# Optimization experiments

Measured on AMD Instinct MI355X. Metric: run time of the kernel, lower is better.

## Reference

```python
import jax, jax.numpy as jnp
import numpy as np

N = 512       # n_nodes (also number of per-node attention heads)
F_IN = 256    # n_feature
H = 64        # h_feature
C = 64        # n_class (must equal H for V * out broadcast)
K = 12        # top-K threshold for learned adjacency
ALPHA = 0.2   # LeakyReLU negative slope


def setup_inputs() -> dict:
    key = jax.random.key(0)
    ks = jax.random.split(key, 6)
    X = jax.random.normal(ks[0], (N, F_IN), jnp.float32)
    # stacked params of the n_nodes first-layer attention heads
    W_stack = jax.random.normal(ks[1], (N, F_IN, H), jnp.float32) * 0.05
    a_stack = jax.random.normal(ks[2], (N, 2 * H, 1), jnp.float32) * 0.05
    # output attention layer: in_Channel = h_feature * n_nodes
    W_out = jax.random.normal(ks[3], (H * N, C), jnp.float32) * 0.02
    a_out = jax.random.normal(ks[4], (2 * C, 1), jnp.float32) * 0.05
    V = jax.random.normal(ks[5], (N, H), jnp.float32) * 0.1
    return {"X": X, "W_stack": W_stack, "a_stack": a_stack,
            "W_out": W_out, "a_out": a_out, "V": V}


def gat_layer(Hx, adj, W, a):
    # Faithful to Graph_Attention_Covlayer.forward, but the O(N^2 * 2F)
    # concat tensor is algebraically collapsed: concat(Wh[i], Wh[j]) @ a
    # == (Wh @ a1)[i] + (Wh @ a2)[j], a broadcast sum.
    Wh = Hx @ W                      # (N, F)
    f = W.shape[1]
    e1 = Wh @ a[:f, 0]               # (N,)
    e2 = Wh @ a[f:, 0]               # (N,)
    S = jax.nn.leaky_relu(e1[:, None] + e2[None, :], ALPHA)  # (N, N)
    A = jax.nn.softmax(S, axis=1)    # softmax BEFORE masking, as in source
    A = jnp.where(adj > 0, A, jnp.zeros_like(A))
    out = A @ Wh                     # (N, F)
    return jax.nn.elu(out)           # concat=True -> elu


def adj_learn(V):
    A = V @ V.T                      # (N, N)
    kth = jax.lax.top_k(A.reshape(-1), K)[0][-1]
    # source: Adj = 1 where A > kth-value, else 0 (strict >)
    return jnp.where(A > kth, jnp.ones_like(A), jnp.zeros_like(A))


def reference(X, W_stack, a_stack, W_out, a_out, V):
    adj = adj_learn(V)
    # all n_nodes heads share input X and adj -> vmap over stacked params
    heads = jax.vmap(lambda W, a: gat_layer(X, adj, W, a))(W_stack, a_stack)  # (N_heads, N, H)
    # torch.cat(..., dim=1): row i = [head0_feats | head1_feats | ...]
    mid = jnp.transpose(heads, (1, 0, 2)).reshape(N, N * H)
    # dropout: eval mode -> identity
    out = gat_layer(mid, adj, W_out, a_out)  # (N, C)
    out = jax.nn.elu(V * out)
    return adj, out
```

## Files before the change

kernel.cpp:

```cpp
#include <hip/hip_runtime.h>


#define CAND_OFF 0
#define XT_OFF   12288
#define KTH_OFF  143360
#define INT_OFF  143424
#define MIDC_OFF 143488
#define PART_OFF 536704

#define H_M    0
#define H_R    1
#define H_ROWS 2
#define H_ER   14
#define H_EJ   26
#define H_ECJ  38

__device__ __forceinline__ float leaky_(float x) { return fmaxf(x, 0.2f * x); }
__device__ __forceinline__ float elu_(float x)   { return x > 0.f ? x : __expf(x) - 1.f; }

__global__ __launch_bounds__(256) void k1_prep(const float* __restrict__ V,
                                               const float* __restrict__ X,
                                               float* __restrict__ wsf,
                                               float* __restrict__ out) {
  int b = blockIdx.x, t = threadIdx.x, l = t & 63, w = t >> 6;
  if (b < 512) {
    __shared__ float vi[64];
    __shared__ float redv[4]; __shared__ int redi[4];
    __shared__ float candv[12]; __shared__ int candi[12];
    if (t < 64) vi[t] = V[b * 64 + t];
    __syncthreads();
    float vr0, vr1;
    {
      const float4* vj = reinterpret_cast<const float4*>(V + t * 64);
      float acc = 0.f;
      #pragma unroll
      for (int q = 0; q < 16; ++q) {
        float4 v4 = vj[q];
        acc += v4.x * vi[q*4] + v4.y * vi[q*4+1] + v4.z * vi[q*4+2] + v4.w * vi[q*4+3];
      }
      vr0 = acc;
    }
    {
      const float4* vj = reinterpret_cast<const float4*>(V + (t + 256) * 64);
      float acc = 0.f;
      #pragma unroll
      for (int q = 0; q < 16; ++q) {
        float4 v4 = vj[q];
        acc += v4.x * vi[q*4] + v4.y * vi[q*4+1] + v4.z * vi[q*4+2] + v4.w * vi[q*4+3];
      }
      vr1 = acc;
    }
    out[b * 512 + t]       = vr0;
    out[b * 512 + 256 + t] = vr1;
    if (b < 128) out[262144 + b * 256 + t] = 0.f;

    float v0 = vr0, v1 = vr1;
    int j0 = t, j1 = t + 256;
    for (int round = 0; round < 12; ++round) {
      float m; int mi;
      if (v0 >= v1) { m = v0; mi = j0; } else { m = v1; mi = j1; }
      #pragma unroll
      for (int d = 1; d < 64; d <<= 1) {
        float ov = __shfl_xor(m, d);
        int   oi = __shfl_xor(mi, d);
        if (ov > m || (ov == m && oi < mi)) { m = ov; mi = oi; }
      }
      if (l == 0) { redv[w] = m; redi[w] = mi; }
      __syncthreads();
      float bm = redv[0]; int bi = redi[0];
      #pragma unroll
      for (int ww = 1; ww < 4; ++ww)
        if (redv[ww] > bm || (redv[ww] == bm && redi[ww] < bi)) { bm = redv[ww]; bi = redi[ww]; }
      if (t == 0) { candv[round] = bm; candi[round] = bi; }
      if (bi == j0) v0 = -INFINITY;
      if (bi == j1) v1 = -INFINITY;
      __syncthreads();
    }
    if (t < 12) {
      float2 c; c.x = candv[t]; c.y = __int_as_float(b * 512 + candi[t]);
      *reinterpret_cast<float2*>(wsf + CAND_OFF + (b * 12 + t) * 2) = c;
    }
  } else {
    __shared__ float tile[64][65];
    int ti = b - 512;
    int tjj = ti & 7;
    int tff = ti >> 3;
    int r = t >> 2, c0 = (t & 3) * 16;
    #pragma unroll
    for (int u = 0; u < 4; ++u) {
      float4 x4 = *reinterpret_cast<const float4*>(X + (tjj*64 + r)*256 + tff*64 + c0 + u*4);
      tile[c0+u*4+0][r] = x4.x; tile[c0+u*4+1][r] = x4.y;
      tile[c0+u*4+2][r] = x4.z; tile[c0+u*4+3][r] = x4.w;
    }
    __syncthreads();
    int fl = t >> 2, jc0 = (t & 3) * 16;
    #pragma unroll
    for (int u = 0; u < 4; ++u) {
      float4 o4 = make_float4(tile[fl][jc0+u*4+0], tile[fl][jc0+u*4+1],
                              tile[fl][jc0+u*4+2], tile[fl][jc0+u*4+3]);
      *reinterpret_cast<float4*>(wsf + XT_OFF + (tff*64 + fl)*512 + tjj*64 + jc0 + u*4) = o4;
    }
  }
}

__global__ void k2_header(float* __restrict__ wsf) {
  __shared__ float redv[4]; __shared__ int redi[4];
  __shared__ float candv[12]; __shared__ int candi[12];
  __shared__ int es_s[12], rows_s[12];
  __shared__ int M_s, R_s;
  int t = threadIdx.x, l = t & 63, w = t >> 6;

  float v[24]; int ix[24];
  const float2* cp = reinterpret_cast<const float2*>(wsf + CAND_OFF);
  #pragma unroll
  for (int k = 0; k < 24; ++k) {
    float2 c = cp[k * 256 + t];
    v[k] = c.x; ix[k] = __float_as_int(c.y);
  }
  unsigned rm = 0;
  for (int round = 0; round < 12; ++round) {
    float m = -INFINITY; int mi = 0x7FFFFFFF; int sel = -1;
    #pragma unroll
    for (int k = 0; k < 24; ++k) {
      bool ok = ((rm >> k) & 1u) == 0u;
      bool better = ok && (v[k] > m || (v[k] == m && ix[k] < mi));
      if (better) { m = v[k]; mi = ix[k]; sel = k; }
    }
    float lm = m; int lmi = mi; (void)lm;
    #pragma unroll
    for (int d = 1; d < 64; d <<= 1) {
      float ov = __shfl_xor(m, d);
      int   oi = __shfl_xor(mi, d);
      if (ov > m || (ov == m && oi < mi)) { m = ov; mi = oi; }
    }
    if (l == 0) { redv[w] = m; redi[w] = mi; }
    __syncthreads();
    float bm = redv[0]; int bi = redi[0];
    #pragma unroll
    for (int ww = 1; ww < 4; ++ww)
      if (redv[ww] > bm || (redv[ww] == bm && redi[ww] < bi)) { bm = redv[ww]; bi = redi[ww]; }
    if (t == 0) { candv[round] = bm; candi[round] = bi; }
    if (sel >= 0 && lmi == bi) rm |= 1u << sel;
    __syncthreads();
  }

  float kv = candv[11];
  bool valid = (t < 12) && (candv[t] > kv);
  int myidx = valid ? candi[t] : 0x7FFFFFFF;
  unsigned long long vm = __ballot(valid);
  if (t < 12) {
    int rank = 0;
    #pragma unroll
    for (int q = 0; q < 12; ++q)
      if (((vm >> q) & 1ull) && candi[q] < myidx) ++rank;
    if (valid) es_s[rank] = myidx;
    if (t == 0) M_s = (int)__popcll(vm & 0xFFFull);
  }
  __syncthreads();
  int M = M_s;
  bool isent = (t < M);
  int i2 = isent ? (es_s[t] >> 9) : -1;
  int j2 = isent ? (es_s[t] & 511) : 0;
  bool isnew = isent && (t == 0 || (es_s[t - 1] >> 9) != i2);
  unsigned long long nm = __ballot(isnew);
  if (isnew) {
    int r = (int)__popcll(nm & ((1ull << t) - 1ull));
    rows_s[r] = i2;
  }
  if (t == 0) R_s = (int)__popcll(nm & 0xFFFull);
  __syncthreads();
  int R = R_s;
  int* ip = (int*)(wsf + INT_OFF);
  if (t == 0) { ip[H_M] = M; ip[H_R] = R; wsf[KTH_OFF] = kv; }
  if (t < 12) {
    ip[H_ROWS + t] = (t < R) ? rows_s[t] : 0;
    int er = 0, ecj = -1;
    if (isent) {
      er = (int)__popcll(nm & ((2ull << t) - 1ull)) - 1;
      for (int r = 0; r < R; ++r) if (rows_s[r] == j2) ecj = r;
    }
    ip[H_ER + t]  = er;
    ip[H_EJ + t]  = isent ? j2 : 0;
    ip[H_ECJ + t] = ecj;
  }
}

__global__ __launch_bounds__(256) void k3_heads(
    const float* __restrict__ X, const float* __restrict__ Wst,
    const float* __restrict__ ast, float* __restrict__ wsf,
    float* __restrict__ out) {
  __shared__ int   shdr[64];
  __shared__ __align__(16) float XeT[3072];
  __shared__ __align__(16) float whp[3072];
  __shared__ float w1l[256], w2l[256];
  __shared__ float e2s[512];
  __shared__ float whl[768];
  __shared__ float e1r[12], mr12[12], sr12[12], av12[12];
  __shared__ float redv[4], redf[48];

  int b = blockIdx.x, t = threadIdx.x, l = t & 63, w = t >> 6;
  const int* ip = (const int*)(wsf + INT_OFF);

  {
    float kv = wsf[KTH_OFF];
    float a0 = out[b * 512 + t], a1 = out[b * 512 + 256 + t];
    out[b * 512 + t]       = (a0 > kv) ? 1.f : 0.f;
    out[b * 512 + 256 + t] = (a1 > kv) ? 1.f : 0.f;
  }
  if (t < 50) shdr[t] = ip[t];
  __syncthreads();
  int M = shdr[H_M], R = shdr[H_R];

  #pragma unroll
  for (int m = 0; m < 12; ++m) {
    float v = 0.f;
    if (m < M) v = X[shdr[H_EJ + m] * 256 + t];
    XeT[t * 12 + m] = v;
  }
  __syncthreads();

  const float* Wb = Wst + b * 16384;
  int fg = l >> 4, kc = (l & 15) << 2;
  float4 a1q = *reinterpret_cast<const float4*>(ast + b * 128 + kc);
  float4 a2q = *reinterpret_cast<const float4*>(ast + b * 128 + 64 + kc);
  float wh[12][4];
  #pragma unroll
  for (int m = 0; m < 12; ++m) { wh[m][0] = wh[m][1] = wh[m][2] = wh[m][3] = 0.f; }

  #pragma unroll 4
  for (int it = 0; it < 16; ++it) {
    int f = w * 64 + it * 4 + fg;
    float4 wq = *reinterpret_cast<const float4*>(Wb + f * 64 + kc);
    float p1 = wq.x*a1q.x + wq.y*a1q.y + wq.z*a1q.z + wq.w*a1q.w;
    float p2 = wq.x*a2q.x + wq.y*a2q.y + wq.z*a2q.z + wq.w*a2q.w;
    #pragma unroll
    for (int d = 1; d < 16; d <<= 1) { p1 += __shfl_xor(p1, d); p2 += __shfl_xor(p2, d); }
    if ((l & 15) == 0) { w1l[f] = p1; w2l[f] = p2; }
    const float4* xr = reinterpret_cast<const float4*>(&XeT[f * 12]);
    float4 xa = xr[0], xb = xr[1], xc = xr[2];
    float xv[12] = { xa.x, xa.y, xa.z, xa.w, xb.x, xb.y, xb.z, xb.w,
                     xc.x, xc.y, xc.z, xc.w };
    #pragma unroll
    for (int m = 0; m < 12; ++m) {
      wh[m][0] += xv[m] * wq.x;
      wh[m][1] += xv[m] * wq.y;
      wh[m][2] += xv[m] * wq.z;
      wh[m][3] += xv[m] * wq.w;
    }
  }
  #pragma unroll
  for (int m = 0; m < 12; ++m) {
    #pragma unroll
    for (int q = 0; q < 4; ++q) {
      float x = wh[m][q];
      x += __shfl_xor(x, 16);
      x += __shfl_xor(x, 32);
      wh[m][q] = x;
    }
  }
  if (l < 16) {
    #pragma unroll
    for (int m = 0; m < 12; ++m) {
      float4 vv = make_float4(wh[m][0], wh[m][1], wh[m][2], wh[m][3]);
      *reinterpret_cast<float4*>(&whp[w * 768 + m * 64 + kc]) = vv;
    }
  }
  __syncthreads();
  #pragma unroll
  for (int c = 0; c < 3; ++c) {
    int o = c * 256 + t;
    whl[o] = whp[o] + whp[768 + o] + whp[1536 + o] + whp[2304 + o];
  }
  for (int r = w; r < R; r += 4) {
    int row = shdr[H_ROWS + r];
    float p = 0.f;
    #pragma unroll
    for (int s = 0; s < 4; ++s) {
      int f = s * 64 + l;
      p += X[row * 256 + f] * w1l[f];
    }
    #pragma unroll
    for (int d = 1; d < 64; d <<= 1) p += __shfl_xor(p, d);
    if (l == 0) e1r[r] = p;
  }
  {
    const float2* XT2 = reinterpret_cast<const float2*>(wsf + XT_OFF);
    float a0 = 0.f, a1 = 0.f;
    #pragma unroll 8
    for (int f = 0; f < 256; ++f) {
      float2 xv = XT2[f * 256 + t];
      float wf = w2l[f];
      a0 += xv.x * wf; a1 += xv.y * wf;
    }
    e2s[2 * t] = a0; e2s[2 * t + 1] = a1;
  }
  __syncthreads();

  {
    float p = fmaxf(e2s[w * 128 + l], e2s[w * 128 + 64 + l]);
    #pragma unroll
    for (int d = 1; d < 64; d <<= 1) p = fmaxf(p, __shfl_xor(p, d));
    if (l == 0) redv[w] = p;
  }
  __syncthreads();
  float maxe2 = fmaxf(fmaxf(redv[0], redv[1]), fmaxf(redv[2], redv[3]));
  for (int r = 0; r < R; ++r) {
    float e1_ = e1r[r];
    float m_ = leaky_(e1_ + maxe2);
    float pe = __expf(leaky_(e1_ + e2s[t]) - m_) + __expf(leaky_(e1_ + e2s[t + 256]) - m_);
    #pragma unroll
    for (int d = 1; d < 64; d <<= 1) pe += __shfl_xor(pe, d);
    if (l == 0) redf[r * 4 + w] = pe;
    if (t == r) mr12[r] = m_;
  }
  __syncthreads();
  if (t < R) sr12[t] = redf[t * 4] + redf[t * 4 + 1] + redf[t * 4 + 2] + redf[t * 4 + 3];
  __syncthreads();
  if (t < M) {
    int r = shdr[H_ER + t];
    av12[t] = __expf(leaky_(e1r[r] + e2s[shdr[H_EJ + t]]) - mr12[r]) / sr12[r];
  }
  __syncthreads();
  for (int r = w; r < R; r += 4) {
    float a = 0.f;
    #pragma unroll
    for (int m = 0; m < 12; ++m) {
      if (m < M && shdr[H_ER + m] == r) a += av12[m] * whl[m * 64 + l];
    }
    wsf[MIDC_OFF + r * 32768 + b * 64 + l] = elu_(a);
  }
}

__global__ void k4_wh2(const float* __restrict__ Wout, float* __restrict__ wsf) {
  __shared__ __align__(16) float midT[256 * 12];
  __shared__ float whp[4][768];
  int b = blockIdx.x, t = threadIdx.x;
  int l = t & 63, w = t >> 6;
  const int* ip = (const int*)(wsf + INT_OFF);
  int R = ip[H_R];
  #pragma unroll
  for (int m = 0; m < 12; ++m) {
    float v = 0.f;
    if (m < R) v = wsf[MIDC_OFF + m * 32768 + b * 256 + t];
    midT[t * 12 + m] = v;
  }
  __syncthreads();
  float acc[12];
  #pragma unroll
  for (int m = 0; m < 12; ++m) acc[m] = 0.f;
  #pragma unroll 2
  for (int ci = 0; ci < 64; ++ci) {
    int cc = w * 64 + ci;
    float wv = Wout[(b * 256 + cc) * 64 + l];
    const float4* xr = reinterpret_cast<const float4*>(&midT[cc * 12]);
    float4 xa = xr[0], xb = xr[1], xc = xr[2];
    acc[0] += xa.x * wv; acc[1] += xa.y * wv; acc[2]  += xa.z * wv; acc[3]  += xa.w * wv;
    acc[4] += xb.x * wv; acc[5] += xb.y * wv; acc[6]  += xb.z * wv; acc[7]  += xb.w * wv;
    acc[8] += xc.x * wv; acc[9] += xc.y * wv; acc[10] += xc.z * wv; acc[11] += xc.w * wv;
  }
  #pragma unroll
  for (int m = 0; m < 12; ++m) whp[w][m * 64 + l] = acc[m];
  __syncthreads();
  #pragma unroll
  for (int c = 0; c < 3; ++c) {
    int o = c * 256 + t;
    float s = whp[0][o] + whp[1][o] + whp[2][o] + whp[3][o];
    wsf[PART_OFF + b * 768 + o] = s;
  }
}

__global__ void k5_final(const float* __restrict__ aout, const float* __restrict__ V,
                         float* __restrict__ wsf, float* __restrict__ out) {
  __shared__ float Wh2[768];
  __shared__ float e1o[12], e2o[12], mr[12], sr[12], avals[12];
  int t = threadIdx.x;
  const int* ip = (const int*)(wsf + INT_OFF);
  int M = ip[H_M], R = ip[H_R];
  for (int o = t, c = 0; c < 3; ++c, o += 256) {
    float s = 0.f;
    #pragma unroll 8
    for (int bb = 0; bb < 128; ++bb) s += wsf[PART_OFF + bb * 768 + o];
    Wh2[o] = s;
  }
  __syncthreads();
  if (t < R) {
    float s1 = 0.f, s2 = 0.f;
    for (int k = 0; k < 64; ++k) {
      float wv = Wh2[t * 64 + k];
      s1 += wv * aout[k];
      s2 += wv * aout[64 + k];
    }
    e1o[t] = s1; e2o[t] = s2;
  }
  __syncthreads();
  if (t < R) {
    float maxe = 0.f;
    for (int r = 0; r < R; ++r) maxe = fmaxf(maxe, e2o[r]);
    float m_ = leaky_(e1o[t] + maxe);
    float s = (float)(512 - R) * __expf(leaky_(e1o[t]) - m_);
    for (int r = 0; r < R; ++r) s += __expf(leaky_(e1o[t] + e2o[r]) - m_);
    mr[t] = m_; sr[t] = s;
  }
  __syncthreads();
  if (t < M) {
    int r = ip[H_ER + t];
    int cj = ip[H_ECJ + t];
    float e2v = (cj >= 0) ? e2o[cj] : 0.f;
    avals[t] = __expf(leaky_(e1o[r] + e2v) - mr[r]) / sr[r];
  }
  __syncthreads();
  int l = t & 63, w = t >> 6;
  for (int r = w; r < R; r += 4) {
    float a = 0.f;
    #pragma unroll
    for (int m = 0; m < 12; ++m) {
      if (m < M && ip[H_ER + m] == r) {
        int cj = ip[H_ECJ + m];
        float wv = (cj >= 0) ? Wh2[cj * 64 + l] : 0.f;
        a += avals[m] * wv;
      }
    }
    int row = ip[H_ROWS + r];
    float o2 = elu_(a);
    out[262144 + row * 64 + l] = elu_(V[row * 64 + l] * o2);
  }
}

extern "C" void kernel_launch(void* const* d_in, const int* in_sizes, int n_in,
                              void* d_out, int out_size, void* d_ws, size_t ws_size,
                              hipStream_t stream) {
  const float* X    = (const float*)d_in[0];
  const float* Wst  = (const float*)d_in[1];
  const float* ast  = (const float*)d_in[2];
  const float* Wout = (const float*)d_in[3];
  const float* aout = (const float*)d_in[4];
  const float* V    = (const float*)d_in[5];
  float* out = (float*)d_out;
  float* wsf = (float*)d_ws;

  k1_prep  <<<544, 256, 0, stream>>>(V, X, wsf, out);
  k2_header<<<1,   256, 0, stream>>>(wsf);
  k3_heads <<<512, 256, 0, stream>>>(X, Wst, ast, wsf, out);
  k4_wh2   <<<128, 256, 0, stream>>>(Wout, wsf);
  k5_final <<<1,   256, 0, stream>>>(aout, V, wsf, out);
}
```

Measured before the change: 142.7 us.

## Precompute head attention projections and e2 GEMM earlier, fuse final kernels via ticket

Moves the per-head W@a projections into extra blocks of the first kernel and computes e2 for all heads as a tiled GEMM alongside the single-block header kernel. This removes the per-block serial 256-step e2 loop and the shuffle reductions from the heads kernel. Top-k candidate selection in k1 drops per-round block syncs by using per-wave candidates merged by one wave. The separate final kernel is folded into k4 through a last-block atomic ticket, saving a launch but adding a threadfence and a larger workspace round trip for the e2 partials.

```diff
diff --git a/kernel.cpp b/kernel.cpp
--- a/kernel.cpp
+++ b/kernel.cpp
@@ -5,28 +5,36 @@
 #define XT_OFF   12288
 #define KTH_OFF  143360
 #define INT_OFF  143424
-#define MIDC_OFF 143488
-#define PART_OFF 536704
-
-#define H_M    0
-#define H_R    1
-#define H_ROWS 2
-#define H_ER   14
-#define H_EJ   26
-#define H_ECJ  38
+#define W1_OFF   143488
+#define W2_OFF   274560
+#define E2P_OFF  405632
+#define MIDC_OFF 1454208
+#define PART_OFF 1847424
+
+#define H_M      0
+#define H_R      1
+#define H_ROWS   2
+#define H_ER     14
+#define H_EJ     26
+#define H_ECJ    38
+#define H_TICKET 60
 
 __device__ __forceinline__ float leaky_(float x) { return fmaxf(x, 0.2f * x); }
 __device__ __forceinline__ float elu_(float x)   { return x > 0.f ? x : __expf(x) - 1.f; }
 
 __global__ __launch_bounds__(256) void k1_prep(const float* __restrict__ V,
                                                const float* __restrict__ X,
+                                               const float* __restrict__ Wst,
+                                               const float* __restrict__ ast,
                                                float* __restrict__ wsf,
                                                float* __restrict__ out) {
+  __shared__ float vi[64];
+  __shared__ float wv[48]; __shared__ int wi[48];
+  __shared__ float tile[64][65];
   int b = blockIdx.x, t = threadIdx.x, l = t & 63, w = t >> 6;
+
   if (b < 512) {
-    __shared__ float vi[64];
-    __shared__ float redv[4]; __shared__ int redi[4];
-    __shared__ float candv[12]; __shared__ int candi[12];
+    if (b == 0 && t == 0) ((int*)(wsf + INT_OFF))[H_TICKET] = 0;
     if (t < 64) vi[t] = V[b * 64 + t];
     __syncthreads();
     float vr0, vr1;
@@ -65,26 +73,32 @@
         int   oi = __shfl_xor(mi, d);
         if (ov > m || (ov == m && oi < mi)) { m = ov; mi = oi; }
       }
-      if (l == 0) { redv[w] = m; redi[w] = mi; }
-      __syncthreads();
-      float bm = redv[0]; int bi = redi[0];
-      #pragma unroll
-      for (int ww = 1; ww < 4; ++ww)
-        if (redv[ww] > bm || (redv[ww] == bm && redi[ww] < bi)) { bm = redv[ww]; bi = redi[ww]; }
-      if (t == 0) { candv[round] = bm; candi[round] = bi; }
-      if (bi == j0) v0 = -INFINITY;
-      if (bi == j1) v1 = -INFINITY;
-      __syncthreads();
-    }
-    if (t < 12) {
-      float2 c; c.x = candv[t]; c.y = __int_as_float(b * 512 + candi[t]);
-      *reinterpret_cast<float2*>(wsf + CAND_OFF + (b * 12 + t) * 2) = c;
-    }
-  } else {
-    __shared__ float tile[64][65];
+      if (l == 0) { wv[w * 12 + round] = m; wi[w * 12 + round] = mi; }
+      if (mi == j0) v0 = -INFINITY;
+      if (mi == j1) v1 = -INFINITY;
+    }
+    __syncthreads();
+    if (w == 0) {
+      float cv = (l < 48) ? wv[l] : -INFINITY;
+      int   ci = (l < 48) ? wi[l] : 0x7FFFFFFF;
+      for (int round = 0; round < 12; ++round) {
+        float m = cv; int mi = ci;
+        #pragma unroll
+        for (int d = 1; d < 64; d <<= 1) {
+          float ov = __shfl_xor(m, d);
+          int   oi = __shfl_xor(mi, d);
+          if (ov > m || (ov == m && oi < mi)) { m = ov; mi = oi; }
+        }
+        if (l == 0) {
+          float2 c; c.x = m; c.y = __int_as_float(b * 512 + mi);
+          *reinterpret_cast<float2*>(wsf + CAND_OFF + (b * 12 + round) * 2) = c;
+        }
+        if (ci == mi) cv = -INFINITY;
+      }
+    }
+  } else if (b < 544) {
     int ti = b - 512;
-    int tjj = ti & 7;
-    int tff = ti >> 3;
+    int tjj = ti & 7, tff = ti >> 3;
     int r = t >> 2, c0 = (t & 3) * 16;
     #pragma unroll
     for (int u = 0; u < 4; ++u) {
@@ -100,15 +114,80 @@
                               tile[fl][jc0+u*4+2], tile[fl][jc0+u*4+3]);
       *reinterpret_cast<float4*>(wsf + XT_OFF + (tff*64 + fl)*512 + tjj*64 + jc0 + u*4) = o4;
     }
+  } else {
+    int h = b - 544;
+    int kc = (t & 15) << 2;
+    float4 a1q = *reinterpret_cast<const float4*>(ast + h * 128 + kc);
+    float4 a2q = *reinterpret_cast<const float4*>(ast + h * 128 + 64 + kc);
+    const float* Wb = Wst + h * 16384;
+    float p1a[16], p2a[16];
+    #pragma unroll
+    for (int it = 0; it < 16; ++it) {
+      float4 wq = *reinterpret_cast<const float4*>(Wb + it * 1024 + t * 4);
+      p1a[it] = wq.x*a1q.x + wq.y*a1q.y + wq.z*a1q.z + wq.w*a1q.w;
+      p2a[it] = wq.x*a2q.x + wq.y*a2q.y + wq.z*a2q.z + wq.w*a2q.w;
+    }
+    #pragma unroll
+    for (int it = 0; it < 16; ++it) {
+      float p1 = p1a[it], p2 = p2a[it];
+      #pragma unroll
+      for (int d = 1; d < 16; d <<= 1) { p1 += __shfl_xor(p1, d); p2 += __shfl_xor(p2, d); }
+      if ((t & 15) == 0) {
+        int f = it * 16 + (t >> 4);
+        wsf[W1_OFF + h * 256 + f] = p1;
+        wsf[W2_OFF + h * 256 + f] = p2;
+      }
+    }
   }
 }
 
-__global__ void k2_header(float* __restrict__ wsf) {
+__global__ __launch_bounds__(256) void k2_e2hdr(const float* __restrict__ X,
+                                                float* __restrict__ wsf) {
+  __shared__ __align__(16) float As[64][68];
+  __shared__ __align__(16) float Bs[64][68];
   __shared__ float redv[4]; __shared__ int redi[4];
   __shared__ float candv[12]; __shared__ int candi[12];
   __shared__ int es_s[12], rows_s[12];
   __shared__ int M_s, R_s;
-  int t = threadIdx.x, l = t & 63, w = t >> 6;
+  int b = blockIdx.x, t = threadIdx.x, l = t & 63, w = t >> 6;
+
+  if (b < 256) {
+    int q = b >> 6, bh = (b >> 3) & 7, bj = b & 7;
+    int r = t >> 2, c0 = (t & 3) * 16;
+    const float* wsrc = wsf + W2_OFF + (bh * 64 + r) * 256 + q * 64 + c0;
+    const float* xsrc = X + (bj * 64 + r) * 256 + q * 64 + c0;
+    #pragma unroll
+    for (int u = 0; u < 4; ++u) {
+      float4 a4 = *reinterpret_cast<const float4*>(wsrc + u * 4);
+      float4 b4 = *reinterpret_cast<const float4*>(xsrc + u * 4);
+      As[c0 + u*4 + 0][r] = a4.x; As[c0 + u*4 + 1][r] = a4.y;
+      As[c0 + u*4 + 2][r] = a4.z; As[c0 + u*4 + 3][r] = a4.w;
+      Bs[c0 + u*4 + 0][r] = b4.x; Bs[c0 + u*4 + 1][r] = b4.y;
+      Bs[c0 + u*4 + 2][r] = b4.z; Bs[c0 + u*4 + 3][r] = b4.w;
+    }
+    __syncthreads();
+    int th = t >> 4, tj = t & 15;
+    float acc[4][4] = {};
+    #pragma unroll 8
+    for (int f = 0; f < 64; ++f) {
+      float4 a4 = *reinterpret_cast<const float4*>(&As[f][th * 4]);
+      float4 b4 = *reinterpret_cast<const float4*>(&Bs[f][tj * 4]);
+      float av[4] = { a4.x, a4.y, a4.z, a4.w };
+      float bv[4] = { b4.x, b4.y, b4.z, b4.w };
+      #pragma unroll
+      for (int i = 0; i < 4; ++i)
+        #pragma unroll
+        for (int j = 0; j < 4; ++j)
+          acc[i][j] += av[i] * bv[j];
+    }
+    float* dst = wsf + E2P_OFF + q * 262144 + (bh * 64 + th * 4) * 512 + bj * 64 + tj * 4;
+    #pragma unroll
+    for (int i = 0; i < 4; ++i) {
+      float4 o4 = make_float4(acc[i][0], acc[i][1], acc[i][2], acc[i][3]);
+      *reinterpret_cast<float4*>(dst + i * 512) = o4;
+    }
+    return;
+  }
 
   float v[24]; int ix[24];
   const float2* cp = reinterpret_cast<const float2*>(wsf + CAND_OFF);
@@ -126,7 +205,7 @@
       bool better = ok && (v[k] > m || (v[k] == m && ix[k] < mi));
       if (better) { m = v[k]; mi = ix[k]; sel = k; }
     }
-    float lm = m; int lmi = mi; (void)lm;
+    int lmi = mi;
     #pragma unroll
     for (int d = 1; d < 64; d <<= 1) {
       float ov = __shfl_xor(m, d);
@@ -143,7 +222,6 @@
     if (sel >= 0 && lmi == bi) rm |= 1u << sel;
     __syncthreads();
   }
-
   float kv = candv[11];
   bool valid = (t < 12) && (candv[t] > kv);
   int myidx = valid ? candi[t] : 0x7FFFFFFF;
@@ -187,12 +265,11 @@
 
 __global__ __launch_bounds__(256) void k3_heads(
     const float* __restrict__ X, const float* __restrict__ Wst,
-    const float* __restrict__ ast, float* __restrict__ wsf,
-    float* __restrict__ out) {
+    float* __restrict__ wsf, float* __restrict__ out) {
   __shared__ int   shdr[64];
   __shared__ __align__(16) float XeT[3072];
   __shared__ __align__(16) float whp[3072];
-  __shared__ float w1l[256], w2l[256];
+  __shared__ float w1l[256];
   __shared__ float e2s[512];
   __shared__ float whl[768];
   __shared__ float e1r[12], mr12[12], sr12[12], av12[12];
@@ -208,6 +285,16 @@
     out[b * 512 + 256 + t] = (a1 > kv) ? 1.f : 0.f;
   }
   if (t < 50) shdr[t] = ip[t];
+  w1l[t] = wsf[W1_OFF + b * 256 + t];
+  {
+    float s0 = 0.f, s1 = 0.f;
+    #pragma unroll
+    for (int q = 0; q < 4; ++q) {
+      s0 += wsf[E2P_OFF + q * 262144 + b * 512 + t];
+      s1 += wsf[E2P_OFF + q * 262144 + b * 512 + 256 + t];
+    }
+    e2s[t] = s0; e2s[t + 256] = s1;
+  }
   __syncthreads();
   int M = shdr[H_M], R = shdr[H_R];
 
@@ -221,21 +308,13 @@
 
   const float* Wb = Wst + b * 16384;
   int fg = l >> 4, kc = (l & 15) << 2;
-  float4 a1q = *reinterpret_cast<const float4*>(ast + b * 128 + kc);
-  float4 a2q = *reinterpret_cast<const float4*>(ast + b * 128 + 64 + kc);
   float wh[12][4];
   #pragma unroll
   for (int m = 0; m < 12; ++m) { wh[m][0] = wh[m][1] = wh[m][2] = wh[m][3] = 0.f; }
-
   #pragma unroll 4
   for (int it = 0; it < 16; ++it) {
     int f = w * 64 + it * 4 + fg;
     float4 wq = *reinterpret_cast<const float4*>(Wb + f * 64 + kc);
-    float p1 = wq.x*a1q.x + wq.y*a1q.y + wq.z*a1q.z + wq.w*a1q.w;
-    float p2 = wq.x*a2q.x + wq.y*a2q.y + wq.z*a2q.z + wq.w*a2q.w;
-    #pragma unroll
-    for (int d = 1; d < 16; d <<= 1) { p1 += __shfl_xor(p1, d); p2 += __shfl_xor(p2, d); }
-    if ((l & 15) == 0) { w1l[f] = p1; w2l[f] = p2; }
     const float4* xr = reinterpret_cast<const float4*>(&XeT[f * 12]);
     float4 xa = xr[0], xb = xr[1], xc = xr[2];
     float xv[12] = { xa.x, xa.y, xa.z, xa.w, xb.x, xb.y, xb.z, xb.w,
@@ -283,17 +362,6 @@
     for (int d = 1; d < 64; d <<= 1) p += __shfl_xor(p, d);
     if (l == 0) e1r[r] = p;
   }
-  {
-    const float2* XT2 = reinterpret_cast<const float2*>(wsf + XT_OFF);
-    float a0 = 0.f, a1 = 0.f;
-    #pragma unroll 8
-    for (int f = 0; f < 256; ++f) {
-      float2 xv = XT2[f * 256 + t];
-      float wf = w2l[f];
-      a0 += xv.x * wf; a1 += xv.y * wf;
-    }
-    e2s[2 * t] = a0; e2s[2 * t + 1] = a1;
-  }
   __syncthreads();
 
   {
@@ -331,13 +399,20 @@
   }
 }
 
-__global__ void k4_wh2(const float* __restrict__ Wout, float* __restrict__ wsf) {
-  __shared__ __align__(16) float midT[256 * 12];
-  __shared__ float whp[4][768];
-  int b = blockIdx.x, t = threadIdx.x;
-  int l = t & 63, w = t >> 6;
-  const int* ip = (const int*)(wsf + INT_OFF);
-  int R = ip[H_R];
+__global__ __launch_bounds__(256) void k4_final(const float* __restrict__ Wout,
+                                                const float* __restrict__ aout,
+                                                const float* __restrict__ V,
+                                                float* __restrict__ wsf,
+                                                float* __restrict__ out) {
+  __shared__ __align__(16) float midT[3072];
+  __shared__ float whp4[4][768];
+  __shared__ float Wh2[768];
+  __shared__ float e1o[12], e2o[12], mr[12], sr[12], avals[12];
+  __shared__ int lastflag;
+  int b = blockIdx.x, t = threadIdx.x, l = t & 63, w = t >> 6;
+  int* ip = (int*)(wsf + INT_OFF);
+  int M = ip[H_M], R = ip[H_R];
+
   #pragma unroll
   for (int m = 0; m < 12; ++m) {
     float v = 0.f;
@@ -359,23 +434,25 @@
     acc[8] += xc.x * wv; acc[9] += xc.y * wv; acc[10] += xc.z * wv; acc[11] += xc.w * wv;
   }
   #pragma unroll
-  for (int m = 0; m < 12; ++m) whp[w][m * 64 + l] = acc[m];
+  for (int m = 0; m < 12; ++m) whp4[w][m * 64 + l] = acc[m];
   __syncthreads();
   #pragma unroll
   for (int c = 0; c < 3; ++c) {
     int o = c * 256 + t;
-    float s = whp[0][o] + whp[1][o] + whp[2][o] + whp[3][o];
+    float s = whp4[0][o] + whp4[1][o] + whp4[2][o] + whp4[3][o];
     wsf[PART_OFF + b * 768 + o] = s;
   }
-}
-
-__global__ void k5_final(const float* __restrict__ aout, const float* __restrict__ V,
-                         float* __restrict__ wsf, float* __restrict__ out) {
-  __shared__ float Wh2[768];
-  __shared__ float e1o[12], e2o[12], mr[12], sr[12], avals[12];
-  int t = threadIdx.x;
-  const int* ip = (const int*)(wsf + INT_OFF);
-  int M = ip[H_M], R = ip[H_R];
+
+  __threadfence();
+  __syncthreads();
+  if (t == 0) {
+    int old = atomicAdd(&ip[H_TICKET], 1);
+    lastflag = (old == 127) ? 1 : 0;
+  }
+  __syncthreads();
+  if (!lastflag) return;
+  __threadfence();
+
   for (int o = t, c = 0; c < 3; ++c, o += 256) {
     float s = 0.f;
     #pragma unroll 8
@@ -409,7 +486,6 @@
     avals[t] = __expf(leaky_(e1o[r] + e2v) - mr[r]) / sr[r];
   }
   __syncthreads();
-  int l = t & 63, w = t >> 6;
   for (int r = w; r < R; r += 4) {
     float a = 0.f;
     #pragma unroll
@@ -438,9 +514,8 @@
   float* out = (float*)d_out;
   float* wsf = (float*)d_ws;
 
-  k1_prep  <<<544, 256, 0, stream>>>(V, X, wsf, out);
-  k2_header<<<1,   256, 0, stream>>>(wsf);
-  k3_heads <<<512, 256, 0, stream>>>(X, Wst, ast, wsf, out);
-  k4_wh2   <<<128, 256, 0, stream>>>(Wout, wsf);
-  k5_final <<<1,   256, 0, stream>>>(aout, V, wsf, out);
+  k1_prep  <<<1056, 256, 0, stream>>>(V, X, Wst, ast, wsf, out);
+  k2_e2hdr <<<257,  256, 0, stream>>>(X, wsf);
+  k3_heads <<<512,  256, 0, stream>>>(X, Wst, wsf, out);
+  k4_final <<<128,  256, 0, stream>>>(Wout, aout, V, wsf, out);
 }
```

After: 140.7 us. About the same (-1.4%).
